# Kernel tuning notes

Hardware: AMD Instinct MI355X
Metric: run time of the kernel (lower is better)

The kernel has to match this reference:

```python
import jax, jax.numpy as jnp
import numpy as np

VOCAB, EMB, HID, LAT, LAYERS = 32000, 512, 1024, 1024, 2
B, T = 16, 128
IN0 = EMB + HID          # layer-0 GRU input size (emb concat syn_z)
OUT_IN = HID + LAT + EMB # out-projection input (use_last_output=True)


def gru_cell(x, h, W_ih, W_hh, b_ih, b_hh):
    # PyTorch GRUCell: gates ordered [r, z, n]
    gi = x @ W_ih.T + b_ih
    gh = h @ W_hh.T + b_hh
    i_r, i_z, i_n = jnp.split(gi, 3, axis=-1)
    h_r, h_z, h_n = jnp.split(gh, 3, axis=-1)
    r = jax.nn.sigmoid(i_r + h_r)
    z = jax.nn.sigmoid(i_z + h_z)
    n = jnp.tanh(i_n + r * h_n)
    return (1.0 - z) * n + z * h


def setup_inputs() -> dict:
    key = jax.random.key(0)
    ks = jax.random.split(key, 16)
    s = 0.02
    return {
        "input_seq": jax.random.randint(ks[0], (B, T), 0, VOCAB),
        "prev_output": jnp.zeros((B, HID), jnp.float32),
        "sem_z": jax.random.normal(ks[1], (B, LAT), jnp.float32),
        "syn_z": jax.random.normal(ks[2], (B, HID), jnp.float32),
        "hidden": jnp.zeros((LAYERS, B, HID), jnp.float32),
        "emb_table": jax.random.normal(ks[3], (VOCAB, EMB), jnp.float32) * s,
        "W_ih0": jax.random.normal(ks[4], (3 * HID, IN0), jnp.float32) * s,
        "W_hh0": jax.random.normal(ks[5], (3 * HID, HID), jnp.float32) * s,
        "b_ih0": jnp.zeros((3 * HID,), jnp.float32),
        "b_hh0": jnp.zeros((3 * HID,), jnp.float32),
        "W_ih1": jax.random.normal(ks[6], (3 * HID, HID), jnp.float32) * s,
        "W_hh1": jax.random.normal(ks[7], (3 * HID, HID), jnp.float32) * s,
        "b_ih1": jnp.zeros((3 * HID,), jnp.float32),
        "b_hh1": jnp.zeros((3 * HID,), jnp.float32),
        "W_out": jax.random.normal(ks[8], (VOCAB, OUT_IN), jnp.float32) * s,
        "b_out": jnp.zeros((VOCAB,), jnp.float32),
    }


def reference(input_seq, prev_output, sem_z, syn_z, hidden, emb_table,
              W_ih0, W_hh0, b_ih0, b_hh0, W_ih1, W_hh1, b_ih1, b_hh1,
              W_out, b_out):
    # dropout=0.0 -> identity; input_feeding=False so prev_output is unused.
    embs = emb_table[input_seq]            # [B, T, E]
    embs_t = jnp.swapaxes(embs, 0, 1)      # [T, B, E]

    def step(h, emb_t):
        x = jnp.concatenate([emb_t, syn_z], axis=1)        # [B, E+H]
        h0 = gru_cell(x, h[0], W_ih0, W_hh0, b_ih0, b_hh0)  # [B, H]
        h1 = gru_cell(h0, h[1], W_ih1, W_hh1, b_ih1, b_hh1)
        pred = jnp.concatenate([h1, sem_z, emb_t], axis=1)  # [B, H+L+E]
        logits = pred @ W_out.T + b_out                     # [B, V]
        scores = jax.nn.log_softmax(logits, axis=-1)
        return jnp.stack([h0, h1]), (scores, logits)

    hidden_f, (scores, logits) = jax.lax.scan(step, hidden, embs_t)
    # scores/logits: [T, B, V]; output = last layer hidden at final step
    return scores, hidden_f, hidden_f[-1], logits
```

## Files before the change

### kernel.cpp

```cpp
#include <hip/hip_runtime.h>

typedef unsigned short u16;
typedef __attribute__((ext_vector_type(8))) short bf16x8;
typedef __attribute__((ext_vector_type(4))) float f32x4;

__device__ __forceinline__ float bf2f(u16 u) {
  union { unsigned u; float f; } v; v.u = ((unsigned)u) << 16; return v.f;
}
__device__ __forceinline__ u16 f2bf(float f) {
  union { float f; unsigned u; } v; v.f = f;
  unsigned r = v.u + 0x7FFFu + ((v.u >> 16) & 1u);
  return (u16)(r >> 16);
}

__device__ __forceinline__ f32x4 ld_sc_x4(const u16* p) {
  f32x4 r;
  asm volatile("global_load_dwordx4 %0, %1, off sc0 sc1"
               : "=v"(r) : "v"(p) : "memory");
  return r;
}
__device__ __forceinline__ float ld_sc_f32(const float* p) {
  float r;
  asm volatile("global_load_dword %0, %1, off sc0 sc1"
               : "=v"(r) : "v"(p) : "memory");
  return r;
}
__device__ __forceinline__ void st_sc_u16(u16* p, unsigned v) {
  asm volatile("global_store_short %0, %1, off sc0 sc1"
               :: "v"(p), "v"(v) : "memory");
}
__device__ __forceinline__ void st_sc_f32(float* p, float v) {
  asm volatile("global_store_dword %0, %1, off sc0 sc1"
               :: "v"(p), "v"(v) : "memory");
}
#define WAIT_VM0() asm volatile("s_waitcnt vmcnt(0)" ::: "memory")

__device__ __forceinline__ int ld_flag(const int* p) {
  return __hip_atomic_load(p, __ATOMIC_RELAXED, __HIP_MEMORY_SCOPE_AGENT);
}
__device__ __forceinline__ void st_flag(int* p, int v) {
  __hip_atomic_store(p, v, __ATOMIC_RELAXED, __HIP_MEMORY_SCOPE_AGENT);
}

constexpr size_t OFF_WCAT  = 0;
constexpr size_t OFF_WSEM  = 98304000;
constexpr size_t OFF_PART  = 98304000;
constexpr size_t OFF_H1ALL = 130000000;
constexpr size_t OFF_GI0   = 163840000;
constexpr size_t OFF_XOUT  = 189005824;
constexpr size_t OFF_H0ALL = 195297280;
constexpr size_t OFF_WIH0E = 199491584;
constexpr size_t OFF_WIH0S = 202637312;
constexpr size_t OFF_WHH0  = 208928768;
constexpr size_t OFF_WIH1  = 215220224;
constexpr size_t OFF_WHH1  = 221511680;
constexpr size_t OFF_SYNB  = 227803136;
constexpr size_t OFF_SEMB  = 228065280;
constexpr size_t OFF_BASE0 = 228327424;
constexpr size_t OFF_BASEO = 229900288;
constexpr size_t OFF_H0IBF = 246284288;
constexpr size_t OFF_H1IBF = 246317056;
constexpr size_t OFF_FLAGS = 246349824;
constexpr size_t OFF_HIDF  = 262144000;
constexpr size_t OFF_LAST  = 262275072;
constexpr size_t OFF_LOGIT = 262340608;

__global__ __launch_bounds__(256) void conv_bf16_k(
    const float* __restrict__ src, u16* __restrict__ dst,
    int rows, int cols8, int sld, int soff, int dld, int doff) {
  int t = blockIdx.x * 256 + threadIdx.x;
  if (t >= rows * cols8) return;
  int r = t / cols8, c = (t - r * cols8) * 8;
  const float* s = src + (size_t)r * sld + soff + c;
  float4 a = *(const float4*)s;
  float4 b = *(const float4*)(s + 4);
  bf16x8 o;
  o[0] = (short)f2bf(a.x); o[1] = (short)f2bf(a.y);
  o[2] = (short)f2bf(a.z); o[3] = (short)f2bf(a.w);
  o[4] = (short)f2bf(b.x); o[5] = (short)f2bf(b.y);
  o[6] = (short)f2bf(b.z); o[7] = (short)f2bf(b.w);
  *(bf16x8*)(dst + (size_t)r * dld + doff + c) = o;
}

__global__ __launch_bounds__(256) void conv_wout_k(
    const float* __restrict__ Wout, u16* __restrict__ WCAT,
    u16* __restrict__ WSEM) {
  int t = blockIdx.x * 256 + threadIdx.x;
  int r = t / 320, c = (t - r * 320) * 8;
  const float* s = Wout + (size_t)r * 2560 + c;
  float4 a = *(const float4*)s;
  float4 b = *(const float4*)(s + 4);
  bf16x8 o;
  o[0] = (short)f2bf(a.x); o[1] = (short)f2bf(a.y);
  o[2] = (short)f2bf(a.z); o[3] = (short)f2bf(a.w);
  o[4] = (short)f2bf(b.x); o[5] = (short)f2bf(b.y);
  o[6] = (short)f2bf(b.z); o[7] = (short)f2bf(b.w);
  u16* dst;
  if (c < 1024)      dst = WCAT + (size_t)r * 1536 + c;
  else if (c < 2048) dst = WSEM + (size_t)r * 1024 + (c - 1024);
  else               dst = WCAT + (size_t)r * 1536 + 1024 + (c - 2048);
  *(bf16x8*)dst = o;
}

__global__ __launch_bounds__(256) void pack_pad_bf16_k(
    const float* __restrict__ src, u16* __restrict__ dst) {
  int t = blockIdx.x * 256 + threadIdx.x;
  int row = t >> 7, c = (t & 127) * 8;
  bf16x8 o = {0, 0, 0, 0, 0, 0, 0, 0};
  if (row < 16) {
    const float* s = src + row * 1024 + c;
    float4 a = *(const float4*)s;
    float4 b = *(const float4*)(s + 4);
    o[0] = (short)f2bf(a.x); o[1] = (short)f2bf(a.y);
    o[2] = (short)f2bf(a.z); o[3] = (short)f2bf(a.w);
    o[4] = (short)f2bf(b.x); o[5] = (short)f2bf(b.y);
    o[6] = (short)f2bf(b.z); o[7] = (short)f2bf(b.w);
  }
  *(bf16x8*)(dst + (size_t)row * 1024 + c) = o;
}

__global__ __launch_bounds__(256) void gather_emb_k(
    const int* __restrict__ seq, const float* __restrict__ table,
    u16* __restrict__ xout) {
  int t0 = blockIdx.x * 256 + threadIdx.x;
  int tb = t0 >> 6, c = (t0 & 63) * 8;
  int tt = tb >> 4, b = tb & 15;
  int tok = seq[b * 128 + tt];
  const float* s = table + (size_t)tok * 512 + c;
  float4 a = *(const float4*)s;
  float4 bb = *(const float4*)(s + 4);
  bf16x8 o;
  o[0] = (short)f2bf(a.x);  o[1] = (short)f2bf(a.y);
  o[2] = (short)f2bf(a.z);  o[3] = (short)f2bf(a.w);
  o[4] = (short)f2bf(bb.x); o[5] = (short)f2bf(bb.y);
  o[6] = (short)f2bf(bb.z); o[7] = (short)f2bf(bb.w);
  *(bf16x8*)(xout + (size_t)tb * 1536 + 1024 + c) = o;
}

__global__ __launch_bounds__(256) void init_h_k(
    const float* __restrict__ hidden, u16* __restrict__ h0b,
    u16* __restrict__ h1b, int* __restrict__ flags) {
  int i = blockIdx.x * 256 + threadIdx.x;
  h0b[i] = f2bf(hidden[i]);
  h1b[i] = f2bf(hidden[16384 + i]);
  if (i < 4096) flags[i] = 0;
}

__device__ __forceinline__ void stage_tile(const u16* src, char* tile,
                                           int tid) {
  f32x4 tmp[8];
#pragma unroll
  for (int q = 0; q < 8; ++q) {
    int c = q * 256 + tid;
    int row = c >> 7, kc = c & 127;
    tmp[q] = ld_sc_x4(src + (size_t)row * 1024 + kc * 8);
  }
  WAIT_VM0();
  __builtin_amdgcn_sched_barrier(0);
#pragma unroll
  for (int q = 0; q < 8; ++q) {
    int c = q * 256 + tid;
    int row = c >> 7, kc = c & 127;
    int byte = (row * 2048 + kc * 16) ^ ((row & 7) << 4);
    *(bf16x8*)(tile + byte) = *(bf16x8*)&tmp[q];
  }
}

__global__ __launch_bounds__(256, 1) void gru_persist3_k(
    const float* __restrict__ hidden, const u16* __restrict__ h0i,
    const u16* __restrict__ h1i, const float* __restrict__ gi0,
    const u16* __restrict__ Whh0, const u16* __restrict__ Wih1,
    const u16* __restrict__ Whh1, const float* __restrict__ bhh0,
    const float* __restrict__ bih1, const float* __restrict__ bhh1,
    u16* __restrict__ h0all, u16* __restrict__ h1all, u16* __restrict__ xout,
    float* __restrict__ part, float* __restrict__ hidf,
    float* __restrict__ last, int* __restrict__ flags) {
  extern __shared__ char ldsb[];
  char* Ab = ldsb + 98304;
  float* Cl = (float*)(ldsb + 131072);
  const int tid = threadIdx.x, bid = blockIdx.x;
  const int wave = tid >> 6, lane = tid & 63;
  const int role = bid >> 6, lb = bid & 63, jb = lb * 16;
  int* f0 = flags, *fih = flags + 1024, *f1 = flags + 2048;

  const u16* Wsrc = role == 0 ? Whh0 : (role == 1 ? Wih1 : Whh1);
  for (int idx = tid; idx < 48 * 128; idx += 256) {
    int row = idx >> 7, c = idx & 127;
    int g = row >> 4, jj2 = row & 15;
    const u16* src = Wsrc + (size_t)(g * 1024 + jb + jj2) * 1024 + c * 8;
    int byte = (row * 2048 + c * 16) ^ ((row & 7) << 4);
    *(bf16x8*)(ldsb + byte) = *(const bf16x8*)src;
  }

  const int eb = tid >> 4, jj = tid & 15, j = jb + jj;
  float hp = 0.f, bR = 0.f, bZ = 0.f, bN = 0.f, iR = 0.f, iZ = 0.f, iN = 0.f;
  if (role == 0) {
    hp = hidden[eb * 1024 + j];
    bR = bhh0[j]; bZ = bhh0[1024 + j]; bN = bhh0[2048 + j];
  } else if (role == 2) {
    hp = hidden[16384 + eb * 1024 + j];
    bR = bhh1[j]; bZ = bhh1[1024 + j]; bN = bhh1[2048 + j];
    iR = bih1[j]; iZ = bih1[1024 + j]; iN = bih1[2048 + j];
  }
  __syncthreads();

  const int arow = lane & 15, aq = lane >> 4;
  for (int t = 0; t < 128; ++t) {
    if (role == 0) {
      if (t > 0 && tid < 64)
        while (ld_flag(f0 + tid * 16) < t) __builtin_amdgcn_s_sleep(1);
    } else if (role == 1) {
      if (tid < 64)
        while (ld_flag(f0 + tid * 16) < t + 1) __builtin_amdgcn_s_sleep(1);
    } else {
      if (t > 0 && tid < 64)
        while (ld_flag(f1 + tid * 16) < t) __builtin_amdgcn_s_sleep(1);
    }
    __syncthreads();

    const u16* asrc;
    if (role == 0)      asrc = t ? h0all + (size_t)(t - 1) * 16384 : h0i;
    else if (role == 1) asrc = h0all + (size_t)t * 16384;
    else                asrc = t ? h1all + (size_t)(t - 1) * 16384 : h1i;
    stage_tile(asrc, Ab, tid);
    __syncthreads();

    {
      f32x4 a0 = {0.f, 0.f, 0.f, 0.f}, a1 = a0, a2 = a0;
#pragma unroll
      for (int i = 0; i < 8; ++i) {
        int ks = wave + i * 4;
        int abyte = (arow * 2048 + ks * 64 + aq * 16) ^ ((arow & 7) << 4);
        bf16x8 af = *(const bf16x8*)(Ab + abyte);
        int r0 = arow, r1 = 16 + arow, r2 = 32 + arow;
        bf16x8 b0 = *(const bf16x8*)(
            ldsb + ((r0 * 2048 + ks * 64 + aq * 16) ^ ((r0 & 7) << 4)));
        bf16x8 b1 = *(const bf16x8*)(
            ldsb + ((r1 * 2048 + ks * 64 + aq * 16) ^ ((r1 & 7) << 4)));
        bf16x8 b2 = *(const bf16x8*)(
            ldsb + ((r2 * 2048 + ks * 64 + aq * 16) ^ ((r2 & 7) << 4)));
        a0 = __builtin_amdgcn_mfma_f32_16x16x32_bf16(af, b0, a0, 0, 0, 0);
        a1 = __builtin_amdgcn_mfma_f32_16x16x32_bf16(af, b1, a1, 0, 0, 0);
        a2 = __builtin_amdgcn_mfma_f32_16x16x32_bf16(af, b2, a2, 0, 0, 0);
      }
#pragma unroll
      for (int r = 0; r < 4; ++r) {
        int ci = (aq * 4 + r) * 16 + arow + aq * 8;
        Cl[(0 * 4 + wave) * 288 + ci] = a0[r];
        Cl[(1 * 4 + wave) * 288 + ci] = a1[r];
        Cl[(2 * 4 + wave) * 288 + ci] = a2[r];
      }
    }
    if (role == 2 && tid == 0)
      while (ld_flag(fih + lb * 16) < t + 1) __builtin_amdgcn_s_sleep(1);
    __syncthreads();

    {
      int ci = eb * 16 + jj + (eb >> 2) * 8;
      float s0 = Cl[0 * 288 + ci] + Cl[1 * 288 + ci] +
                 Cl[2 * 288 + ci] + Cl[3 * 288 + ci];
      float s1 = Cl[4 * 288 + ci] + Cl[5 * 288 + ci] +
                 Cl[6 * 288 + ci] + Cl[7 * 288 + ci];
      float s2 = Cl[8 * 288 + ci] + Cl[9 * 288 + ci] +
                 Cl[10 * 288 + ci] + Cl[11 * 288 + ci];
      if (role == 1) {
        float* pp = part + ((size_t)t * 64 + lb) * 768 + eb * 16 + jj;
        st_sc_f32(pp, s0);
        st_sc_f32(pp + 256, s1);
        st_sc_f32(pp + 512, s2);
        WAIT_VM0();
      } else {
        float ir, iz, inn;
        if (role == 0) {
          const float* g = gi0 + ((size_t)t * 16 + eb) * 3072 + j;
          ir = g[0]; iz = g[1024]; inn = g[2048];
        } else {
          const float* pp = part + ((size_t)t * 64 + lb) * 768 + eb * 16 + jj;
          float p0 = ld_sc_f32(pp), p1 = ld_sc_f32(pp + 256),
                p2 = ld_sc_f32(pp + 512);
          WAIT_VM0();
          __builtin_amdgcn_sched_barrier(0);
          ir = p0 + iR; iz = p1 + iZ; inn = p2 + iN;
        }
        float r = 1.f / (1.f + __expf(-(ir + s0 + bR)));
        float z = 1.f / (1.f + __expf(-(iz + s1 + bZ)));
        float n = tanhf(inn + r * (s2 + bN));
        float hnew = (1.f - z) * n + z * hp;
        hp = hnew;
        u16 hb = f2bf(hnew);
        if (role == 0) {
          st_sc_u16(h0all + ((size_t)t * 16 + eb) * 1024 + j, (unsigned)hb);
          if (t == 127) hidf[eb * 1024 + j] = hnew;
        } else {
          st_sc_u16(h1all + ((size_t)t * 16 + eb) * 1024 + j, (unsigned)hb);
          xout[((size_t)t * 16 + eb) * 1536 + j] = hb;
          if (t == 127) {
            hidf[16384 + eb * 1024 + j] = hnew;
            last[eb * 1024 + j] = hnew;
          }
        }
        WAIT_VM0();
      }
    }
    __syncthreads();
    if (tid == 0) {
      if (role == 0)      st_flag(f0 + lb * 16, t + 1);
      else if (role == 1) st_flag(fih + lb * 16, t + 1);
      else                st_flag(f1 + lb * 16, t + 1);
    }
  }
}

template <int MODE>
__global__ __launch_bounds__(256) void gemm_bt_k(
    const u16* __restrict__ A, int lda, const u16* __restrict__ Bw, int ldb,
    float* __restrict__ C, int ldc, const float* __restrict__ add,
    int N, int K) {
  __shared__ u16 Asm_[128 * 32];
  __shared__ u16 Bsm_[128 * 32];
  const int m0 = blockIdx.x * 128, n0 = blockIdx.y * 128;
  const int tid = threadIdx.x, wave = tid >> 6, lane = tid & 63;
  const int wm = (wave >> 1) * 64, wn = (wave & 1) * 64;
  const int lrow = lane & 15, lk = (lane >> 4) * 8;
  f32x4 acc[4][4] = {};
  for (int k0 = 0; k0 < K; k0 += 32) {
    __syncthreads();
#pragma unroll
    for (int q = 0; q < 2; ++q) {
      int c = (wave * 2 + q) * 64 + lane;
      int row = c >> 2, seg = c & 3;
      const u16* src = A + (size_t)(m0 + row) * lda + k0 + seg * 8;
      u16* dst = Asm_ + (wave * 2 + q) * 512;
      __builtin_amdgcn_global_load_lds(
          (const __attribute__((address_space(1))) void*)src,
          (__attribute__((address_space(3))) void*)dst, 16, 0, 0);
    }
#pragma unroll
    for (int q = 0; q < 2; ++q) {
      int c = (wave * 2 + q) * 64 + lane;
      int row = c >> 2, seg = c & 3;
      const u16* src = Bw + (size_t)(n0 + row) * ldb + k0 + seg * 8;
      u16* dst = Bsm_ + (wave * 2 + q) * 512;
      __builtin_amdgcn_global_load_lds(
          (const __attribute__((address_space(1))) void*)src,
          (__attribute__((address_space(3))) void*)dst, 16, 0, 0);
    }
    asm volatile("s_waitcnt vmcnt(0)" ::: "memory");
    __syncthreads();
    bf16x8 af[4], bfr[4];
#pragma unroll
    for (int i = 0; i < 4; ++i) {
      af[i]  = *(const bf16x8*)(Asm_ + (wm + i * 16 + lrow) * 32 + lk);
      bfr[i] = *(const bf16x8*)(Bsm_ + (wn + i * 16 + lrow) * 32 + lk);
    }
#pragma unroll
    for (int i = 0; i < 4; ++i)
#pragma unroll
      for (int jx = 0; jx < 4; ++jx)
        acc[i][jx] = __builtin_amdgcn_mfma_f32_16x16x32_bf16(
            af[i], bfr[jx], acc[i][jx], 0, 0, 0);
  }
  const int lr4 = (lane >> 4) * 4;
#pragma unroll
  for (int i = 0; i < 4; ++i) {
#pragma unroll
    for (int jx = 0; jx < 4; ++jx) {
      int gc = n0 + wn + jx * 16 + lrow;
#pragma unroll
      for (int r = 0; r < 4; ++r) {
        int gr = m0 + wm + i * 16 + lr4 + r;
        float v = acc[i][jx][r];
        if (MODE == 1) v += add[(gr & 15) * N + gc];
        else if (MODE == 2) v += add[gc];
        C[(size_t)gr * ldc + gc] = v;
      }
    }
  }
}

template <int MODE, bool SWZ>
__global__ __launch_bounds__(512) void gemm256_bt_k(
    const u16* __restrict__ A, int lda, const u16* __restrict__ Bw, int ldb,
    float* __restrict__ C, int ldc, const float* __restrict__ add,
    int N, int K) {
  __shared__ u16 Asm_[256 * 32];
  __shared__ u16 Bsm_[128 * 32];
  int bx = blockIdx.x, by = blockIdx.y;
  if (SWZ) {
    int nx = gridDim.x;
    int orig = by * nx + bx;
    int cpx = (nx * gridDim.y) >> 3;
    int wg = (orig & 7) * cpx + (orig >> 3);
    bx = wg % nx; by = wg / nx;
  }
  const int m0 = bx * 256, n0 = by * 128;
  const int tid = threadIdx.x, wave = tid >> 6, lane = tid & 63;
  const int wm = (wave >> 1) * 64, wn = (wave & 1) * 64;
  const int lrow = lane & 15, lk = (lane >> 4) * 8;
  f32x4 acc[4][4] = {};
  for (int k0 = 0; k0 < K; k0 += 32) {
    __syncthreads();
#pragma unroll
    for (int q = 0; q < 2; ++q) {
      int c = (q * 8 + wave) * 64 + lane;
      int row = c >> 2, seg = c & 3;
      const u16* src = A + (size_t)(m0 + row) * lda + k0 + seg * 8;
      u16* dst = Asm_ + (q * 8 + wave) * 512;
      __builtin_amdgcn_global_load_lds(
          (const __attribute__((address_space(1))) void*)src,
          (__attribute__((address_space(3))) void*)dst, 16, 0, 0);
    }
    {
      int c = wave * 64 + lane;
      int row = c >> 2, seg = c & 3;
      const u16* src = Bw + (size_t)(n0 + row) * ldb + k0 + seg * 8;
      u16* dst = Bsm_ + wave * 512;
      __builtin_amdgcn_global_load_lds(
          (const __attribute__((address_space(1))) void*)src,
          (__attribute__((address_space(3))) void*)dst, 16, 0, 0);
    }
    asm volatile("s_waitcnt vmcnt(0)" ::: "memory");
    __syncthreads();
    bf16x8 af[4], bfr[4];
#pragma unroll
    for (int i = 0; i < 4; ++i) {
      af[i]  = *(const bf16x8*)(Asm_ + (wm + i * 16 + lrow) * 32 + lk);
      bfr[i] = *(const bf16x8*)(Bsm_ + (wn + i * 16 + lrow) * 32 + lk);
    }
#pragma unroll
    for (int i = 0; i < 4; ++i)
#pragma unroll
      for (int jx = 0; jx < 4; ++jx)
        acc[i][jx] = __builtin_amdgcn_mfma_f32_16x16x32_bf16(
            af[i], bfr[jx], acc[i][jx], 0, 0, 0);
  }
  const int lr4 = (lane >> 4) * 4;
#pragma unroll
  for (int i = 0; i < 4; ++i) {
#pragma unroll
    for (int jx = 0; jx < 4; ++jx) {
      int gc = n0 + wn + jx * 16 + lrow;
#pragma unroll
      for (int r = 0; r < 4; ++r) {
        int gr = m0 + wm + i * 16 + lr4 + r;
        float v = acc[i][jx][r];
        if (MODE == 1) v += add[(gr & 15) * N + gc];
        else if (MODE == 2) v += add[gc];
        C[(size_t)gr * ldc + gc] = v;
      }
    }
  }
}

__global__ __launch_bounds__(256) void log_softmax_k(
    const float* __restrict__ logits, float* __restrict__ scores) {
  int row = blockIdx.x;
  const float* x = logits + (size_t)row * 32000;
  float* y = scores + (size_t)row * 32000;
  __shared__ float redm[4], reds[4];
  int tid = threadIdx.x;
  float m = -3.4e38f, s = 0.f;
  for (int idx = tid * 4; idx < 32000; idx += 1024) {
    float4 v = *(const float4*)(x + idx);
    float cm = fmaxf(fmaxf(v.x, v.y), fmaxf(v.z, v.w));
    if (cm > m) { s *= __expf(m - cm); m = cm; }
    s += __expf(v.x - m) + __expf(v.y - m) + __expf(v.z - m) + __expf(v.w - m);
  }
  for (int off = 1; off < 64; off <<= 1) {
    float mo = __shfl_xor(m, off), so = __shfl_xor(s, off);
    float nm = fmaxf(m, mo);
    s = s * __expf(m - nm) + so * __expf(mo - nm);
    m = nm;
  }
  if ((tid & 63) == 0) { redm[tid >> 6] = m; reds[tid >> 6] = s; }
  __syncthreads();
  {
    float fm = fmaxf(fmaxf(redm[0], redm[1]), fmaxf(redm[2], redm[3]));
    float fs = reds[0] * __expf(redm[0] - fm) + reds[1] * __expf(redm[1] - fm) +
               reds[2] * __expf(redm[2] - fm) + reds[3] * __expf(redm[3] - fm);
    float lse = fm + logf(fs);
    for (int idx = tid * 4; idx < 32000; idx += 1024) {
      float4 v = *(const float4*)(x + idx);
      float4 o;
      o.x = v.x - lse; o.y = v.y - lse; o.z = v.z - lse; o.w = v.w - lse;
      *(float4*)(y + idx) = o;
    }
  }
}

extern "C" void kernel_launch(void* const* d_in, const int* in_sizes, int n_in,
                              void* d_out, int out_size, void* d_ws,
                              size_t ws_size, hipStream_t stream) {
  const int*   seq    = (const int*)d_in[0];
  const float* sem    = (const float*)d_in[2];
  const float* syn    = (const float*)d_in[3];
  const float* hidden = (const float*)d_in[4];
  const float* table  = (const float*)d_in[5];
  const float* Wih0   = (const float*)d_in[6];
  const float* Whh0   = (const float*)d_in[7];
  const float* bih0   = (const float*)d_in[8];
  const float* bhh0   = (const float*)d_in[9];
  const float* Wih1   = (const float*)d_in[10];
  const float* Whh1   = (const float*)d_in[11];
  const float* bih1   = (const float*)d_in[12];
  const float* bhh1   = (const float*)d_in[13];
  const float* Wout   = (const float*)d_in[14];
  const float* bout   = (const float*)d_in[15];

  char* base = (char*)d_out;
  float* scores = (float*)base;
  u16*   WCAT   = (u16*)(base + OFF_WCAT);
  u16*   WSEM   = (u16*)(base + OFF_WSEM);
  float* PART   = (float*)(base + OFF_PART);
  u16*   H1ALL  = (u16*)(base + OFF_H1ALL);
  float* GI0    = (float*)(base + OFF_GI0);
  u16*   XOUT   = (u16*)(base + OFF_XOUT);
  u16*   H0ALL  = (u16*)(base + OFF_H0ALL);
  u16*   WIH0E  = (u16*)(base + OFF_WIH0E);
  u16*   WIH0S  = (u16*)(base + OFF_WIH0S);
  u16*   WHH0B  = (u16*)(base + OFF_WHH0);
  u16*   WIH1B  = (u16*)(base + OFF_WIH1);
  u16*   WHH1B  = (u16*)(base + OFF_WHH1);
  u16*   SYNB   = (u16*)(base + OFF_SYNB);
  u16*   SEMB   = (u16*)(base + OFF_SEMB);
  float* BASE0  = (float*)(base + OFF_BASE0);
  float* BASEO  = (float*)(base + OFF_BASEO);
  u16*   H0IBF  = (u16*)(base + OFF_H0IBF);
  u16*   H1IBF  = (u16*)(base + OFF_H1IBF);
  int*   FLAGS  = (int*)(base + OFF_FLAGS);
  float* hidf   = (float*)(base + OFF_HIDF);
  float* last   = (float*)(base + OFF_LAST);
  float* logits = (float*)(base + OFF_LOGIT);

  conv_wout_k<<<40000, 256, 0, stream>>>(Wout, WCAT, WSEM);
  conv_bf16_k<<<768, 256, 0, stream>>>(Wih0, WIH0E, 3072, 64, 1536, 0, 512, 0);
  conv_bf16_k<<<1536, 256, 0, stream>>>(Wih0, WIH0S, 3072, 128, 1536, 512, 1024, 0);
  conv_bf16_k<<<1536, 256, 0, stream>>>(Whh0, WHH0B, 3072, 128, 1024, 0, 1024, 0);
  conv_bf16_k<<<1536, 256, 0, stream>>>(Wih1, WIH1B, 3072, 128, 1024, 0, 1024, 0);
  conv_bf16_k<<<1536, 256, 0, stream>>>(Whh1, WHH1B, 3072, 128, 1024, 0, 1024, 0);

  gather_emb_k<<<512, 256, 0, stream>>>(seq, table, XOUT);
  pack_pad_bf16_k<<<64, 256, 0, stream>>>(syn, SYNB);
  pack_pad_bf16_k<<<64, 256, 0, stream>>>(sem, SEMB);
  init_h_k<<<64, 256, 0, stream>>>(hidden, H0IBF, H1IBF, FLAGS);

  gemm_bt_k<2><<<dim3(1, 24), 256, 0, stream>>>(
      SYNB, 1024, WIH0S, 1024, BASE0, 3072, bih0, 3072, 1024);
  gemm_bt_k<2><<<dim3(1, 250), 256, 0, stream>>>(
      SEMB, 1024, WSEM, 1024, BASEO, 32000, bout, 32000, 1024);

  gemm256_bt_k<1, true><<<dim3(8, 24), 512, 0, stream>>>(
      XOUT + 1024, 1536, WIH0E, 512, GI0, 3072, BASE0, 3072, 512);

  hipFuncSetAttribute((const void*)gru_persist3_k,
                      hipFuncAttributeMaxDynamicSharedMemorySize, 145408);
  gru_persist3_k<<<192, 256, 145408, stream>>>(
      hidden, H0IBF, H1IBF, GI0, WHH0B, WIH1B, WHH1B, bhh0, bih1, bhh1,
      H0ALL, H1ALL, XOUT, PART, hidf, last, FLAGS);

  gemm256_bt_k<1, true><<<dim3(8, 250), 512, 0, stream>>>(
      XOUT, 1536, WCAT, 1536, logits, 32000, BASEO, 32000, 1536);

  log_softmax_k<<<2048, 256, 0, stream>>>(logits, scores);
}
```

Baseline: 1.136 ms.

## Merge weight-conversion and init launches; double-buffer LDS in GEMM kernels

Five separate recurrent-weight conversion launches become one kernel that routes by column chunk, and the syn/sem packing plus hidden/flag init become one launch. This cuts launch overhead and inter-kernel gaps. Both GEMM kernels now double-buffer their LDS tiles, issuing the next K-slice's global-to-LDS loads before the MFMAs on the current slice. The cost is twice the shared memory per block, which may lower occupancy.

```diff
diff --git a/kernel.cpp b/kernel.cpp
--- a/kernel.cpp
+++ b/kernel.cpp
@@ -65,13 +65,32 @@
 constexpr size_t OFF_LAST  = 262275072;
 constexpr size_t OFF_LOGIT = 262340608;
 
-__global__ __launch_bounds__(256) void conv_bf16_k(
-    const float* __restrict__ src, u16* __restrict__ dst,
-    int rows, int cols8, int sld, int soff, int dld, int doff) {
+__global__ __launch_bounds__(256) void conv_recw_k(
+    const float* __restrict__ Wih0, const float* __restrict__ Whh0,
+    const float* __restrict__ Wih1, const float* __restrict__ Whh1,
+    u16* __restrict__ WIH0E, u16* __restrict__ WIH0S, u16* __restrict__ WHH0B,
+    u16* __restrict__ WIH1B, u16* __restrict__ WHH1B) {
   int t = blockIdx.x * 256 + threadIdx.x;
-  if (t >= rows * cols8) return;
-  int r = t / cols8, c = (t - r * cols8) * 8;
-  const float* s = src + (size_t)r * sld + soff + c;
+  if (t >= 3072 * 576) return;
+  int r = t / 576, c = t - r * 576;
+  const float* s;
+  u16* d;
+  if (c < 64) {
+    s = Wih0 + (size_t)r * 1536 + c * 8;
+    d = WIH0E + (size_t)r * 512 + c * 8;
+  } else if (c < 192) {
+    s = Wih0 + (size_t)r * 1536 + 512 + (c - 64) * 8;
+    d = WIH0S + (size_t)r * 1024 + (c - 64) * 8;
+  } else if (c < 320) {
+    s = Whh0 + (size_t)r * 1024 + (c - 192) * 8;
+    d = WHH0B + (size_t)r * 1024 + (c - 192) * 8;
+  } else if (c < 448) {
+    s = Wih1 + (size_t)r * 1024 + (c - 320) * 8;
+    d = WIH1B + (size_t)r * 1024 + (c - 320) * 8;
+  } else {
+    s = Whh1 + (size_t)r * 1024 + (c - 448) * 8;
+    d = WHH1B + (size_t)r * 1024 + (c - 448) * 8;
+  }
   float4 a = *(const float4*)s;
   float4 b = *(const float4*)(s + 4);
   bf16x8 o;
@@ -79,7 +98,7 @@
   o[2] = (short)f2bf(a.z); o[3] = (short)f2bf(a.w);
   o[4] = (short)f2bf(b.x); o[5] = (short)f2bf(b.y);
   o[6] = (short)f2bf(b.z); o[7] = (short)f2bf(b.w);
-  *(bf16x8*)(dst + (size_t)r * dld + doff + c) = o;
+  *(bf16x8*)d = o;
 }
 
 __global__ __launch_bounds__(256) void conv_wout_k(
@@ -102,21 +121,34 @@
   *(bf16x8*)dst = o;
 }
 
-__global__ __launch_bounds__(256) void pack_pad_bf16_k(
-    const float* __restrict__ src, u16* __restrict__ dst) {
-  int t = blockIdx.x * 256 + threadIdx.x;
-  int row = t >> 7, c = (t & 127) * 8;
-  bf16x8 o = {0, 0, 0, 0, 0, 0, 0, 0};
-  if (row < 16) {
-    const float* s = src + row * 1024 + c;
-    float4 a = *(const float4*)s;
-    float4 b = *(const float4*)(s + 4);
-    o[0] = (short)f2bf(a.x); o[1] = (short)f2bf(a.y);
-    o[2] = (short)f2bf(a.z); o[3] = (short)f2bf(a.w);
-    o[4] = (short)f2bf(b.x); o[5] = (short)f2bf(b.y);
-    o[6] = (short)f2bf(b.z); o[7] = (short)f2bf(b.w);
-  }
-  *(bf16x8*)(dst + (size_t)row * 1024 + c) = o;
+__global__ __launch_bounds__(256) void small_init_k(
+    const float* __restrict__ syn, const float* __restrict__ sem,
+    const float* __restrict__ hidden, u16* __restrict__ SYNB,
+    u16* __restrict__ SEMB, u16* __restrict__ h0b, u16* __restrict__ h1b,
+    int* __restrict__ flags) {
+  int bb = blockIdx.x;
+  if (bb < 128) {
+    const float* src = bb < 64 ? syn : sem;
+    u16* dst = bb < 64 ? SYNB : SEMB;
+    int t = (bb & 63) * 256 + threadIdx.x;
+    int row = t >> 7, c = (t & 127) * 8;
+    bf16x8 o = {0, 0, 0, 0, 0, 0, 0, 0};
+    if (row < 16) {
+      const float* s = src + row * 1024 + c;
+      float4 a = *(const float4*)s;
+      float4 b = *(const float4*)(s + 4);
+      o[0] = (short)f2bf(a.x); o[1] = (short)f2bf(a.y);
+      o[2] = (short)f2bf(a.z); o[3] = (short)f2bf(a.w);
+      o[4] = (short)f2bf(b.x); o[5] = (short)f2bf(b.y);
+      o[6] = (short)f2bf(b.z); o[7] = (short)f2bf(b.w);
+    }
+    *(bf16x8*)(dst + (size_t)row * 1024 + c) = o;
+  } else {
+    int i = (bb - 128) * 256 + threadIdx.x;
+    h0b[i] = f2bf(hidden[i]);
+    h1b[i] = f2bf(hidden[16384 + i]);
+    if (i < 4096) flags[i] = 0;
+  }
 }
 
 __global__ __launch_bounds__(256) void gather_emb_k(
@@ -135,15 +167,6 @@
   o[4] = (short)f2bf(bb.x); o[5] = (short)f2bf(bb.y);
   o[6] = (short)f2bf(bb.z); o[7] = (short)f2bf(bb.w);
   *(bf16x8*)(xout + (size_t)tb * 1536 + 1024 + c) = o;
-}
-
-__global__ __launch_bounds__(256) void init_h_k(
-    const float* __restrict__ hidden, u16* __restrict__ h0b,
-    u16* __restrict__ h1b, int* __restrict__ flags) {
-  int i = blockIdx.x * 256 + threadIdx.x;
-  h0b[i] = f2bf(hidden[i]);
-  h1b[i] = f2bf(hidden[16384 + i]);
-  if (i < 4096) flags[i] = 0;
 }
 
 __device__ __forceinline__ void stage_tile(const u16* src, char* tile,
@@ -316,21 +339,20 @@
     const u16* __restrict__ A, int lda, const u16* __restrict__ Bw, int ldb,
     float* __restrict__ C, int ldc, const float* __restrict__ add,
     int N, int K) {
-  __shared__ u16 Asm_[128 * 32];
-  __shared__ u16 Bsm_[128 * 32];
+  __shared__ u16 Asm_[2][128 * 32];
+  __shared__ u16 Bsm_[2][128 * 32];
   const int m0 = blockIdx.x * 128, n0 = blockIdx.y * 128;
   const int tid = threadIdx.x, wave = tid >> 6, lane = tid & 63;
   const int wm = (wave >> 1) * 64, wn = (wave & 1) * 64;
   const int lrow = lane & 15, lk = (lane >> 4) * 8;
-  f32x4 acc[4][4] = {};
-  for (int k0 = 0; k0 < K; k0 += 32) {
-    __syncthreads();
+
+  auto STAGE = [&](int buf, int k0) {
 #pragma unroll
     for (int q = 0; q < 2; ++q) {
       int c = (wave * 2 + q) * 64 + lane;
       int row = c >> 2, seg = c & 3;
       const u16* src = A + (size_t)(m0 + row) * lda + k0 + seg * 8;
-      u16* dst = Asm_ + (wave * 2 + q) * 512;
+      u16* dst = Asm_[buf] + (wave * 2 + q) * 512;
       __builtin_amdgcn_global_load_lds(
           (const __attribute__((address_space(1))) void*)src,
           (__attribute__((address_space(3))) void*)dst, 16, 0, 0);
@@ -340,18 +362,26 @@
       int c = (wave * 2 + q) * 64 + lane;
       int row = c >> 2, seg = c & 3;
       const u16* src = Bw + (size_t)(n0 + row) * ldb + k0 + seg * 8;
-      u16* dst = Bsm_ + (wave * 2 + q) * 512;
+      u16* dst = Bsm_[buf] + (wave * 2 + q) * 512;
       __builtin_amdgcn_global_load_lds(
           (const __attribute__((address_space(1))) void*)src,
           (__attribute__((address_space(3))) void*)dst, 16, 0, 0);
     }
+  };
+
+  const int nIt = K >> 5;
+  STAGE(0, 0);
+  f32x4 acc[4][4] = {};
+  for (int it = 0; it < nIt; ++it) {
+    const int cur = it & 1;
     asm volatile("s_waitcnt vmcnt(0)" ::: "memory");
     __syncthreads();
+    if (it + 1 < nIt) STAGE(cur ^ 1, (it + 1) * 32);
     bf16x8 af[4], bfr[4];
 #pragma unroll
     for (int i = 0; i < 4; ++i) {
-      af[i]  = *(const bf16x8*)(Asm_ + (wm + i * 16 + lrow) * 32 + lk);
-      bfr[i] = *(const bf16x8*)(Bsm_ + (wn + i * 16 + lrow) * 32 + lk);
+      af[i]  = *(const bf16x8*)(Asm_[cur] + (wm + i * 16 + lrow) * 32 + lk);
+      bfr[i] = *(const bf16x8*)(Bsm_[cur] + (wn + i * 16 + lrow) * 32 + lk);
     }
 #pragma unroll
     for (int i = 0; i < 4; ++i)
@@ -383,8 +413,8 @@
     const u16* __restrict__ A, int lda, const u16* __restrict__ Bw, int ldb,
     float* __restrict__ C, int ldc, const float* __restrict__ add,
     int N, int K) {
-  __shared__ u16 Asm_[256 * 32];
-  __shared__ u16 Bsm_[128 * 32];
+  __shared__ u16 Asm_[2][256 * 32];
+  __shared__ u16 Bsm_[2][128 * 32];
   int bx = blockIdx.x, by = blockIdx.y;
   if (SWZ) {
     int nx = gridDim.x;
@@ -397,15 +427,14 @@
   const int tid = threadIdx.x, wave = tid >> 6, lane = tid & 63;
   const int wm = (wave >> 1) * 64, wn = (wave & 1) * 64;
   const int lrow = lane & 15, lk = (lane >> 4) * 8;
-  f32x4 acc[4][4] = {};
-  for (int k0 = 0; k0 < K; k0 += 32) {
-    __syncthreads();
+
+  auto STAGE = [&](int buf, int k0) {
 #pragma unroll
     for (int q = 0; q < 2; ++q) {
       int c = (q * 8 + wave) * 64 + lane;
       int row = c >> 2, seg = c & 3;
       const u16* src = A + (size_t)(m0 + row) * lda + k0 + seg * 8;
-      u16* dst = Asm_ + (q * 8 + wave) * 512;
+      u16* dst = Asm_[buf] + (q * 8 + wave) * 512;
       __builtin_amdgcn_global_load_lds(
           (const __attribute__((address_space(1))) void*)src,
           (__attribute__((address_space(3))) void*)dst, 16, 0, 0);
@@ -414,18 +443,26 @@
       int c = wave * 64 + lane;
       int row = c >> 2, seg = c & 3;
       const u16* src = Bw + (size_t)(n0 + row) * ldb + k0 + seg * 8;
-      u16* dst = Bsm_ + wave * 512;
+      u16* dst = Bsm_[buf] + wave * 512;
       __builtin_amdgcn_global_load_lds(
           (const __attribute__((address_space(1))) void*)src,
           (__attribute__((address_space(3))) void*)dst, 16, 0, 0);
     }
+  };
+
+  const int nIt = K >> 5;
+  STAGE(0, 0);
+  f32x4 acc[4][4] = {};
+  for (int it = 0; it < nIt; ++it) {
+    const int cur = it & 1;
     asm volatile("s_waitcnt vmcnt(0)" ::: "memory");
     __syncthreads();
+    if (it + 1 < nIt) STAGE(cur ^ 1, (it + 1) * 32);
     bf16x8 af[4], bfr[4];
 #pragma unroll
     for (int i = 0; i < 4; ++i) {
-      af[i]  = *(const bf16x8*)(Asm_ + (wm + i * 16 + lrow) * 32 + lk);
-      bfr[i] = *(const bf16x8*)(Bsm_ + (wn + i * 16 + lrow) * 32 + lk);
+      af[i]  = *(const bf16x8*)(Asm_[cur] + (wm + i * 16 + lrow) * 32 + lk);
+      bfr[i] = *(const bf16x8*)(Bsm_[cur] + (wn + i * 16 + lrow) * 32 + lk);
     }
 #pragma unroll
     for (int i = 0; i < 4; ++i)
@@ -533,16 +570,12 @@
   float* logits = (float*)(base + OFF_LOGIT);
 
   conv_wout_k<<<40000, 256, 0, stream>>>(Wout, WCAT, WSEM);
-  conv_bf16_k<<<768, 256, 0, stream>>>(Wih0, WIH0E, 3072, 64, 1536, 0, 512, 0);
-  conv_bf16_k<<<1536, 256, 0, stream>>>(Wih0, WIH0S, 3072, 128, 1536, 512, 1024, 0);
-  conv_bf16_k<<<1536, 256, 0, stream>>>(Whh0, WHH0B, 3072, 128, 1024, 0, 1024, 0);
-  conv_bf16_k<<<1536, 256, 0, stream>>>(Wih1, WIH1B, 3072, 128, 1024, 0, 1024, 0);
-  conv_bf16_k<<<1536, 256, 0, stream>>>(Whh1, WHH1B, 3072, 128, 1024, 0, 1024, 0);
+  conv_recw_k<<<6912, 256, 0, stream>>>(
+      Wih0, Whh0, Wih1, Whh1, WIH0E, WIH0S, WHH0B, WIH1B, WHH1B);
 
   gather_emb_k<<<512, 256, 0, stream>>>(seq, table, XOUT);
-  pack_pad_bf16_k<<<64, 256, 0, stream>>>(syn, SYNB);
-  pack_pad_bf16_k<<<64, 256, 0, stream>>>(sem, SEMB);
-  init_h_k<<<64, 256, 0, stream>>>(hidden, H0IBF, H1IBF, FLAGS);
+  small_init_k<<<192, 256, 0, stream>>>(
+      syn, sem, hidden, SYNB, SEMB, H0IBF, H1IBF, FLAGS);
 
   gemm_bt_k<2><<<dim3(1, 24), 256, 0, stream>>>(
       SYNB, 1024, WIH0S, 1024, BASE0, 3072, bih0, 3072, 1024);
```

After: 1.092 ms. 3.9% less time.
